# Performance work log

Hardware: AMD Instinct MI355X
Metric: run time of the kernel (lower is better)

## Reference

```python
import jax, jax.numpy as jnp
import numpy as np

B, T, H, W = 2, 4, 32, 32
DINO_DIM, COG_DIM, NUM_HEADS = 768, 1920, 12
HEAD_DIM = DINO_DIM // NUM_HEADS


def _layernorm(x, g, b, eps=1e-5):
    mu = jnp.mean(x, axis=-1, keepdims=True)
    var = jnp.mean(jnp.square(x - mu), axis=-1, keepdims=True)
    return (x - mu) * jax.lax.rsqrt(var + eps) * g + b


def setup_inputs() -> dict:
    key = jax.random.key(0)
    ks = jax.random.split(key, 12)
    s_d = 1.0 / np.sqrt(DINO_DIM)
    s_c = 1.0 / np.sqrt(COG_DIM)
    return {
        "dino_query": jax.random.normal(ks[0], (B, DINO_DIM, H, W), jnp.float32),
        "cogvideo_keys": jax.random.normal(ks[1], (B, T, H, W, COG_DIM), jnp.float32),
        "temporal_weights": jax.random.uniform(ks[2], (T,), jnp.float32),
        "Wq": jax.random.normal(ks[3], (DINO_DIM, DINO_DIM), jnp.float32) * s_d,
        "bq": jnp.zeros((DINO_DIM,), jnp.float32),
        "Wk": jax.random.normal(ks[4], (COG_DIM, DINO_DIM), jnp.float32) * s_c,
        "bk": jnp.zeros((DINO_DIM,), jnp.float32),
        "Wv": jax.random.normal(ks[5], (COG_DIM, DINO_DIM), jnp.float32) * s_c,
        "bv": jnp.zeros((DINO_DIM,), jnp.float32),
        "Wo": jax.random.normal(ks[6], (DINO_DIM, DINO_DIM), jnp.float32) * s_d,
        "bo": jnp.zeros((DINO_DIM,), jnp.float32),
        "gq": jnp.ones((DINO_DIM,), jnp.float32),
        "Bq": jnp.zeros((DINO_DIM,), jnp.float32),
        "gkv": jnp.ones((COG_DIM,), jnp.float32),
        "Bkv": jnp.zeros((COG_DIM,), jnp.float32),
    }


def reference(dino_query, cogvideo_keys, temporal_weights,
              Wq, bq, Wk, bk, Wv, bv, Wo, bo, gq, Bq, gkv, Bkv):
    b, c, h, w = dino_query.shape
    t = cogvideo_keys.shape[1]
    hw, tkv = h * w, t * cogvideo_keys.shape[2] * cogvideo_keys.shape[3]

    # [B,C,H,W] -> [B,H,W,C]; project after LayerNorm
    xq = _layernorm(jnp.transpose(dino_query, (0, 2, 3, 1)), gq, Bq)
    xkv = _layernorm(cogvideo_keys, gkv, Bkv)
    q = xq @ Wq + bq                      # [B,H,W,C]
    k = xkv @ Wk + bk                     # [B,T,Hk,Wk,C]
    v = xkv @ Wv + bv

    q = q.reshape(b, hw, NUM_HEADS, HEAD_DIM).transpose(0, 2, 1, 3)    # [B,nh,HW,hd]
    k = k.reshape(b, tkv, NUM_HEADS, HEAD_DIM).transpose(0, 2, 1, 3)   # [B,nh,TKV,hd]
    v = v.reshape(b, tkv, NUM_HEADS, HEAD_DIM).transpose(0, 2, 1, 3)

    scores = jnp.einsum('bnqd,bnkd->bnqk', q, k) / np.sqrt(HEAD_DIM)   # [B,nh,HW,TKV]
    # per-key temporal weight: each of the T frames contributes HW keys
    w_key = jnp.repeat(temporal_weights, tkv // t)                     # [TKV]
    scores = scores * w_key[None, None, None, :]
    probs = jax.nn.softmax(scores, axis=-1)

    out = jnp.einsum('bnqk,bnkd->bnqd', probs, v)                      # [B,nh,HW,hd]
    out = out.transpose(0, 2, 1, 3).reshape(b, h, w, c)
    out = out @ Wo + bo
    return jnp.transpose(out, (0, 3, 1, 2))                            # [B,C,H,W]
```

## Files before the change

kernel.cpp:

```cpp
#include <hip/hip_runtime.h>
#include <hip/hip_bf16.h>
#include <math.h>

#define BB   2
#define HWl  1024
#define DINO 768
#define COG  1920
#define NHh  12
#define TKV  4096
#define MQ   (BB*HWl)
#define MKV  (BB*TKV)
#define NSPL 4
#define ROWS_PER_SPLIT (BB*NHh*HWl)

typedef __attribute__((ext_vector_type(8))) short bf16x8;
typedef __attribute__((ext_vector_type(4))) float f32x4;

__device__ __forceinline__ unsigned short f2bf_bits(float f) {
    __hip_bfloat16 h = __float2bfloat16(f);
    return *reinterpret_cast<unsigned short*>(&h);
}

__device__ __forceinline__ void glds16(const __hip_bfloat16* g, __hip_bfloat16* l) {
    __builtin_amdgcn_global_load_lds((const __attribute__((address_space(1))) void*)g,
                                     (__attribute__((address_space(3))) void*)l, 16, 0, 0);
}

__global__ void transpose_dino(const float* __restrict__ x, float* __restrict__ y) {
    int h0 = blockIdx.x * 64, c0 = blockIdx.y * 64, b = blockIdx.z;
    __shared__ float T[64][65];
    #pragma unroll
    for (int i = 0; i < 16; ++i) {
        int idx = threadIdx.x + i * 256;
        int c = idx >> 6, h = idx & 63;
        T[c][h] = x[((size_t)b * DINO + c0 + c) * HWl + h0 + h];
    }
    __syncthreads();
    #pragma unroll
    for (int i = 0; i < 16; ++i) {
        int idx = threadIdx.x + i * 256;
        int r = idx >> 6, c = idx & 63;
        y[((size_t)b * HWl + h0 + r) * DINO + c0 + c] = T[c][r];
    }
}

template<int W, int NC>
__global__ void ln_rows_w(const float* __restrict__ x, const float* __restrict__ g,
                          const float* __restrict__ be, __hip_bfloat16* __restrict__ y) {
    const int W4 = W >> 2;
    int row = blockIdx.x * 4 + (threadIdx.x >> 6);
    int lane = threadIdx.x & 63;
    const float4* xr = (const float4*)(x + (size_t)row * W);
    const float4* g4 = (const float4*)g;
    const float4* b4 = (const float4*)be;
    float4 v[NC];
    float s = 0.f, ss = 0.f;
    #pragma unroll
    for (int i = 0; i < NC; ++i) {
        int c = lane + i * 64;
        float4 t = (c < W4) ? xr[c] : (float4){0.f, 0.f, 0.f, 0.f};
        v[i] = t;
        s  += t.x + t.y + t.z + t.w;
        ss += t.x * t.x + t.y * t.y + t.z * t.z + t.w * t.w;
    }
    #pragma unroll
    for (int off = 1; off < 64; off <<= 1) {
        s  += __shfl_xor(s, off);
        ss += __shfl_xor(ss, off);
    }
    float mu = s / W;
    float rstd = rsqrtf(ss / W - mu * mu + 1e-5f);
    ushort4* yr = (ushort4*)(y + (size_t)row * W);
    #pragma unroll
    for (int i = 0; i < NC; ++i) {
        int c = lane + i * 64;
        if (c < W4) {
            float4 t = v[i];
            float4 gg = g4[c], bb = b4[c];
            ushort4 o;
            o.x = f2bf_bits((t.x - mu) * rstd * gg.x + bb.x);
            o.y = f2bf_bits((t.y - mu) * rstd * gg.y + bb.y);
            o.z = f2bf_bits((t.z - mu) * rstd * gg.z + bb.z);
            o.w = f2bf_bits((t.w - mu) * rstd * gg.w + bb.w);
            yr[c] = o;
        }
    }
}

__global__ void wt_trans(const float* __restrict__ Wq, const float* __restrict__ Wk,
                         const float* __restrict__ Wv, const float* __restrict__ Wo,
                         __hip_bfloat16* WqT, __hip_bfloat16* WkvT, __hip_bfloat16* WoT) {
    int mid = blockIdx.z;
    const float* src = (mid == 0) ? Wq : (mid == 1) ? Wk : (mid == 2) ? Wv : Wo;
    __hip_bfloat16* dst;
    int rowoff = 0;
    if (mid == 0) dst = WqT;
    else if (mid == 1) dst = WkvT;
    else if (mid == 2) { dst = WkvT; rowoff = 768; }
    else dst = WoT;
    int K = (mid == 1 || mid == 2) ? COG : DINO;
    int k0 = blockIdx.x * 32;
    if (k0 >= K) return;
    int n0 = blockIdx.y * 32;
    __shared__ float T[32][33];
    #pragma unroll
    for (int i = 0; i < 4; ++i) {
        int idx = threadIdx.x + i * 256;
        int r = idx >> 5, c = idx & 31;
        T[r][c] = src[(size_t)(k0 + r) * DINO + n0 + c];
    }
    __syncthreads();
    #pragma unroll
    for (int i = 0; i < 4; ++i) {
        int idx = threadIdx.x + i * 256;
        int r = idx >> 5, c = idx & 31;
        dst[(size_t)(rowoff + n0 + r) * K + k0 + c] = __float2bfloat16(T[c][r]);
    }
}

__global__ __launch_bounds__(256) void gemm_kv(const __hip_bfloat16* __restrict__ A,
                                               const __hip_bfloat16* __restrict__ Bt,
                                               const float* __restrict__ bk,
                                               const float* __restrict__ bv,
                                               __hip_bfloat16* __restrict__ kb,
                                               __hip_bfloat16* __restrict__ VT) {
    const int K = COG;
    __shared__ __hip_bfloat16 As[128 * 64];
    __shared__ __hip_bfloat16 Bs[128 * 64];
    int m0 = blockIdx.x * 128, n0 = blockIdx.y * 128;
    int tid = threadIdx.x, w = tid >> 6, lane = tid & 63;
    int l4 = lane & 15, lq = lane >> 4;
    int mq = (w & 1) * 64, nq = (w >> 1) * 64;
    f32x4 acc[4][4];
    #pragma unroll
    for (int i = 0; i < 4; ++i)
        #pragma unroll
        for (int j = 0; j < 4; ++j) acc[i][j] = (f32x4){0.f, 0.f, 0.f, 0.f};

    int rr = tid >> 3;
    int gc = (tid & 7) ^ (rr & 7);
    const __hip_bfloat16* ag = A  + (size_t)(m0 + rr) * K + gc * 8;
    const __hip_bfloat16* bg = Bt + (size_t)(n0 + rr) * K + gc * 8;
    __hip_bfloat16* asl = As + (w * 8) * 64;
    __hip_bfloat16* bsl = Bs + (w * 8) * 64;
    int sws = l4 & 7;

    for (int k0 = 0; k0 < K; k0 += 64) {
        __syncthreads();
        #pragma unroll
        for (int g = 0; g < 4; ++g) {
            glds16(ag + (size_t)(g * 32) * K + k0, asl + g * 32 * 64);
            glds16(bg + (size_t)(g * 32) * K + k0, bsl + g * 32 * 64);
        }
        __syncthreads();
        #pragma unroll
        for (int h = 0; h < 2; ++h) {
            bf16x8 a[4], b[4];
            #pragma unroll
            for (int i = 0; i < 4; ++i)
                a[i] = *(const bf16x8*)(As + (mq + 16 * i + l4) * 64 + (((h * 4 + lq) ^ sws) * 8));
            #pragma unroll
            for (int j = 0; j < 4; ++j)
                b[j] = *(const bf16x8*)(Bs + (nq + 16 * j + l4) * 64 + (((h * 4 + lq) ^ sws) * 8));
            #pragma unroll
            for (int i = 0; i < 4; ++i)
                #pragma unroll
                for (int j = 0; j < 4; ++j)
                    acc[i][j] = __builtin_amdgcn_mfma_f32_16x16x32_bf16(a[i], b[j], acc[i][j], 0, 0, 0);
        }
    }

    if (n0 < 768) {
        #pragma unroll
        for (int i = 0; i < 4; ++i)
            #pragma unroll
            for (int j = 0; j < 4; ++j)
                #pragma unroll
                for (int r = 0; r < 4; ++r) {
                    int m = m0 + mq + 16 * i + lq * 4 + r;
                    int n = n0 + nq + 16 * j + l4;
                    kb[(size_t)m * DINO + n] = __float2bfloat16(acc[i][j][r] + bk[n]);
                }
    } else {
        #pragma unroll
        for (int i = 0; i < 4; ++i)
            #pragma unroll
            for (int j = 0; j < 4; ++j)
                #pragma unroll
                for (int r = 0; r < 4; ++r) {
                    int m = m0 + mq + 16 * i + lq * 4 + r;
                    int n = n0 + nq + 16 * j + l4 - 768;
                    VT[((size_t)((m >> 12) * 768 + n)) * TKV + (m & 4095)] =
                        __float2bfloat16(acc[i][j][r] + bv[n]);
                }
    }
}

template<bool ONCHW>
__global__ __launch_bounds__(256) void gemm_qo(const __hip_bfloat16* __restrict__ A,
                                               const __hip_bfloat16* __restrict__ Bt,
                                               const float* __restrict__ bias,
                                               void* __restrict__ outp) {
    const int K = DINO;
    __shared__ __hip_bfloat16 As[64 * 64];
    __shared__ __hip_bfloat16 Bs[128 * 64];
    int m0 = blockIdx.x * 64, n0 = blockIdx.y * 128;
    int tid = threadIdx.x, w = tid >> 6, lane = tid & 63;
    int l4 = lane & 15, lq = lane >> 4;
    int mq = (w & 1) * 32, nq = (w >> 1) * 64;
    f32x4 acc[2][4];
    #pragma unroll
    for (int i = 0; i < 2; ++i)
        #pragma unroll
        for (int j = 0; j < 4; ++j) acc[i][j] = (f32x4){0.f, 0.f, 0.f, 0.f};

    int rr = tid >> 3;
    int gc = (tid & 7) ^ (rr & 7);
    const __hip_bfloat16* ag = A  + (size_t)(m0 + rr) * K + gc * 8;
    const __hip_bfloat16* bg = Bt + (size_t)(n0 + rr) * K + gc * 8;
    __hip_bfloat16* asl = As + (w * 8) * 64;
    __hip_bfloat16* bsl = Bs + (w * 8) * 64;
    int sws = l4 & 7;

    for (int k0 = 0; k0 < K; k0 += 64) {
        __syncthreads();
        #pragma unroll
        for (int g = 0; g < 2; ++g)
            glds16(ag + (size_t)(g * 32) * K + k0, asl + g * 32 * 64);
        #pragma unroll
        for (int g = 0; g < 4; ++g)
            glds16(bg + (size_t)(g * 32) * K + k0, bsl + g * 32 * 64);
        __syncthreads();
        #pragma unroll
        for (int h = 0; h < 2; ++h) {
            bf16x8 a[2], b[4];
            #pragma unroll
            for (int i = 0; i < 2; ++i)
                a[i] = *(const bf16x8*)(As + (mq + 16 * i + l4) * 64 + (((h * 4 + lq) ^ sws) * 8));
            #pragma unroll
            for (int j = 0; j < 4; ++j)
                b[j] = *(const bf16x8*)(Bs + (nq + 16 * j + l4) * 64 + (((h * 4 + lq) ^ sws) * 8));
            #pragma unroll
            for (int i = 0; i < 2; ++i)
                #pragma unroll
                for (int j = 0; j < 4; ++j)
                    acc[i][j] = ONCHW
                      ? __builtin_amdgcn_mfma_f32_16x16x32_bf16(b[j], a[i], acc[i][j], 0, 0, 0)
                      : __builtin_amdgcn_mfma_f32_16x16x32_bf16(a[i], b[j], acc[i][j], 0, 0, 0);
        }
    }

    if (!ONCHW) {
        __hip_bfloat16* out = (__hip_bfloat16*)outp;
        #pragma unroll
        for (int i = 0; i < 2; ++i)
            #pragma unroll
            for (int j = 0; j < 4; ++j)
                #pragma unroll
                for (int r = 0; r < 4; ++r) {
                    int m = m0 + mq + 16 * i + lq * 4 + r;
                    int n = n0 + nq + 16 * j + l4;
                    out[(size_t)m * DINO + n] = __float2bfloat16(acc[i][j][r] + bias[n]);
                }
    } else {
        float* out = (float*)outp;
        #pragma unroll
        for (int i = 0; i < 2; ++i)
            #pragma unroll
            for (int j = 0; j < 4; ++j)
                #pragma unroll
                for (int r = 0; r < 4; ++r) {
                    int n = n0 + nq + 16 * j + lq * 4 + r;
                    int m = m0 + mq + 16 * i + l4;
                    int b = m >> 10, hw = m & 1023;
                    out[((size_t)b * DINO + n) * HWl + hw] = acc[i][j][r] + bias[n];
                }
    }
}

__global__ __launch_bounds__(256) void attn3(const __hip_bfloat16* __restrict__ qb,
                                             const __hip_bfloat16* __restrict__ kb,
                                             const __hip_bfloat16* __restrict__ VT,
                                             const float* __restrict__ tw,
                                             float* __restrict__ Opart,
                                             float* __restrict__ lpart) {
    int bid = blockIdx.x;
    int g = bid % 96, qc = bid / 96;
    int s = g & 3, bh = g >> 2;
    int head = bh % NHh, b = bh / NHh;
    int tid = threadIdx.x, w = tid >> 6, lane = tid & 63;
    int l4 = lane & 15, lq = lane >> 4;

    __shared__ __hip_bfloat16 Ks[64 * 64];
    __shared__ __hip_bfloat16 Vs[64 * 64];
    __shared__ __hip_bfloat16 Ps[4 * 32 * 64];

    const __hip_bfloat16* qbase = qb + (size_t)(b * HWl + qc * 128 + w * 32 + l4) * DINO + head * 64;
    bf16x8 qA0 = *(const bf16x8*)(qbase + lq * 8);
    bf16x8 qA1 = *(const bf16x8*)(qbase + 32 + lq * 8);
    const __hip_bfloat16* qbase2 = qbase + (size_t)16 * DINO;
    bf16x8 qB0 = *(const bf16x8*)(qbase2 + lq * 8);
    bf16x8 qB1 = *(const bf16x8*)(qbase2 + 32 + lq * 8);

    float c = tw[s] * 0.125f * 1.44269504f;
    float l_iA = 0.f, l_iB = 0.f;
    f32x4 oA[4], oB[4];
    #pragma unroll
    for (int j = 0; j < 4; ++j) { oA[j] = (f32x4){0.f,0.f,0.f,0.f}; oB[j] = (f32x4){0.f,0.f,0.f,0.f}; }

    int rowA = w * 16 + (lane >> 3);
    int cg = (lane & 7) ^ ((lane >> 3) & 7);
    const __hip_bfloat16* kg0 = kb + (size_t)(b * TKV + s * 1024 + rowA) * DINO + head * 64 + cg * 8;
    const __hip_bfloat16* kg1 = kg0 + (size_t)8 * DINO;
    const __hip_bfloat16* vg0 = VT + (size_t)(b * 768 + head * 64 + rowA) * TKV + s * 1024 + cg * 8;
    const __hip_bfloat16* vg1 = vg0 + (size_t)8 * TKV;
    __hip_bfloat16* kl0 = Ks + (w * 2 + 0) * 512;
    __hip_bfloat16* kl1 = Ks + (w * 2 + 1) * 512;
    __hip_bfloat16* vl0 = Vs + (w * 2 + 0) * 512;
    __hip_bfloat16* vl1 = Vs + (w * 2 + 1) * 512;

    int sw0 = (lq ^ (l4 & 7)) * 8;
    int sw1 = ((4 + lq) ^ (l4 & 7)) * 8;
    __hip_bfloat16* PsA = Ps + w * 2048 + l4 * 64;
    __hip_bfloat16* PsB = Ps + w * 2048 + (16 + l4) * 64;

    for (int kt = 0; kt < 16; ++kt) {
        __syncthreads();
        glds16(kg0 + (size_t)kt * 64 * DINO, kl0);
        glds16(kg1 + (size_t)kt * 64 * DINO, kl1);
        glds16(vg0 + kt * 64, vl0);
        glds16(vg1 + kt * 64, vl1);
        __syncthreads();

        f32x4 stA[4], stB[4];
        #pragma unroll
        for (int j = 0; j < 4; ++j) {
            const __hip_bfloat16* kr = Ks + (16 * j + l4) * 64;
            bf16x8 kf0 = *(const bf16x8*)(kr + sw0);
            bf16x8 kf1 = *(const bf16x8*)(kr + sw1);
            f32x4 a = (f32x4){0.f,0.f,0.f,0.f};
            a = __builtin_amdgcn_mfma_f32_16x16x32_bf16(kf0, qA0, a, 0, 0, 0);
            a = __builtin_amdgcn_mfma_f32_16x16x32_bf16(kf1, qA1, a, 0, 0, 0);
            stA[j] = a;
            f32x4 bb = (f32x4){0.f,0.f,0.f,0.f};
            bb = __builtin_amdgcn_mfma_f32_16x16x32_bf16(kf0, qB0, bb, 0, 0, 0);
            bb = __builtin_amdgcn_mfma_f32_16x16x32_bf16(kf1, qB1, bb, 0, 0, 0);
            stB[j] = bb;
        }

        float lsA = 0.f, lsB = 0.f;
        #pragma unroll
        for (int j = 0; j < 4; ++j)
            #pragma unroll
            for (int r = 0; r < 4; ++r) {
                float eA = exp2f(stA[j][r] * c);
                float eB = exp2f(stB[j][r] * c);
                stA[j][r] = eA; lsA += eA;
                stB[j][r] = eB; lsB += eB;
            }
        lsA += __shfl_xor(lsA, 16); lsA += __shfl_xor(lsA, 32);
        lsB += __shfl_xor(lsB, 16); lsB += __shfl_xor(lsB, 32);
        l_iA += lsA; l_iB += lsB;

        #pragma unroll
        for (int j = 0; j < 4; ++j) {
            int off = (((2 * j + (lq >> 1)) ^ (l4 & 7)) << 3) + (lq & 1) * 4;
            ushort4 pA, pB;
            pA.x = f2bf_bits(stA[j][0]); pA.y = f2bf_bits(stA[j][1]);
            pA.z = f2bf_bits(stA[j][2]); pA.w = f2bf_bits(stA[j][3]);
            pB.x = f2bf_bits(stB[j][0]); pB.y = f2bf_bits(stB[j][1]);
            pB.z = f2bf_bits(stB[j][2]); pB.w = f2bf_bits(stB[j][3]);
            *(ushort4*)&PsA[off] = pA;
            *(ushort4*)&PsB[off] = pB;
        }
        bf16x8 paA0 = *(const bf16x8*)(PsA + sw0);
        bf16x8 paA1 = *(const bf16x8*)(PsA + sw1);
        bf16x8 paB0 = *(const bf16x8*)(PsB + sw0);
        bf16x8 paB1 = *(const bf16x8*)(PsB + sw1);

        #pragma unroll
        for (int j = 0; j < 4; ++j) {
            const __hip_bfloat16* vr = Vs + (16 * j + l4) * 64;
            bf16x8 vf0 = *(const bf16x8*)(vr + sw0);
            bf16x8 vf1 = *(const bf16x8*)(vr + sw1);
            oA[j] = __builtin_amdgcn_mfma_f32_16x16x32_bf16(paA0, vf0, oA[j], 0, 0, 0);
            oA[j] = __builtin_amdgcn_mfma_f32_16x16x32_bf16(paA1, vf1, oA[j], 0, 0, 0);
            oB[j] = __builtin_amdgcn_mfma_f32_16x16x32_bf16(paB0, vf0, oB[j], 0, 0, 0);
            oB[j] = __builtin_amdgcn_mfma_f32_16x16x32_bf16(paB1, vf1, oB[j], 0, 0, 0);
        }
    }

    size_t rb = (size_t)s * ROWS_PER_SPLIT + (size_t)(b * NHh + head) * HWl + qc * 128 + w * 32;
    #pragma unroll
    for (int j = 0; j < 4; ++j)
        #pragma unroll
        for (int r = 0; r < 4; ++r) {
            Opart[(rb + lq * 4 + r) * 64 + j * 16 + l4]      = oA[j][r];
            Opart[(rb + 16 + lq * 4 + r) * 64 + j * 16 + l4] = oB[j][r];
        }
    if (lq == 0) {
        lpart[rb + l4]      = l_iA;
        lpart[rb + 16 + l4] = l_iB;
    }
}

__global__ void combine(const float* __restrict__ Opart, const float* __restrict__ lpart,
                        __hip_bfloat16* __restrict__ attn) {
    int p = blockIdx.x * 4 + (threadIdx.x >> 6);
    int d = threadIdx.x & 63;
    float L = 0.f, O = 0.f;
    #pragma unroll
    for (int s = 0; s < NSPL; ++s) {
        L += lpart[(size_t)s * ROWS_PER_SPLIT + p];
        O += Opart[((size_t)s * ROWS_PER_SPLIT + p) * 64 + d];
    }
    float res = O / L;
    int q = p & 1023;
    int bh = p >> 10;
    int head = bh % NHh, b = bh / NHh;
    attn[((size_t)(b * HWl + q)) * DINO + head * 64 + d] = __float2bfloat16(res);
}

extern "C" void kernel_launch(void* const* d_in, const int* in_sizes, int n_in,
                              void* d_out, int out_size, void* d_ws, size_t ws_size,
                              hipStream_t stream) {
    (void)in_sizes; (void)n_in; (void)out_size; (void)ws_size;
    const float* dino = (const float*)d_in[0];
    const float* cog  = (const float*)d_in[1];
    const float* tw   = (const float*)d_in[2];
    const float* Wq   = (const float*)d_in[3];
    const float* bq   = (const float*)d_in[4];
    const float* Wk   = (const float*)d_in[5];
    const float* bk   = (const float*)d_in[6];
    const float* Wv   = (const float*)d_in[7];
    const float* bv   = (const float*)d_in[8];
    const float* Wo   = (const float*)d_in[9];
    const float* bo   = (const float*)d_in[10];
    const float* gq   = (const float*)d_in[11];
    const float* Bq   = (const float*)d_in[12];
    const float* gkv  = (const float*)d_in[13];
    const float* Bkv  = (const float*)d_in[14];

    char* p = (char*)d_ws;
    float* xqT = (float*)p;                    p += (size_t)MQ * DINO * 4;
    __hip_bfloat16* xq = (__hip_bfloat16*)p;   p += (size_t)MQ * DINO * 2;
    char* alias = p;                           p += (size_t)MKV * COG * 2;
    __hip_bfloat16* xkv = (__hip_bfloat16*)alias;
    __hip_bfloat16* WqT  = (__hip_bfloat16*)p; p += (size_t)DINO * DINO * 2;
    __hip_bfloat16* WkvT = (__hip_bfloat16*)p; p += (size_t)1536 * COG * 2;
    __hip_bfloat16* WoT  = (__hip_bfloat16*)p; p += (size_t)DINO * DINO * 2;
    __hip_bfloat16* qb   = (__hip_bfloat16*)p; p += (size_t)MQ  * DINO * 2;
    __hip_bfloat16* kb   = (__hip_bfloat16*)p; p += (size_t)MKV * DINO * 2;
    __hip_bfloat16* VT   = (__hip_bfloat16*)p; p += (size_t)MKV * DINO * 2;
    __hip_bfloat16* attnb = (__hip_bfloat16*)p; p += (size_t)MQ * DINO * 2;
    float* Opart = (float*)alias;
    float* lpart = (float*)(alias + (size_t)NSPL * ROWS_PER_SPLIT * 64 * 4);

    transpose_dino<<<dim3(16, 12, 2), 256, 0, stream>>>(dino, xqT);
    ln_rows_w<DINO, 3><<<MQ / 4,  256, 0, stream>>>(xqT, gq, Bq, xq);
    ln_rows_w<COG,  8><<<MKV / 4, 256, 0, stream>>>(cog, gkv, Bkv, xkv);
    wt_trans<<<dim3(60, 24, 4), 256, 0, stream>>>(Wq, Wk, Wv, Wo, WqT, WkvT, WoT);

    gemm_qo<false><<<dim3(32, 6), 256, 0, stream>>>(xq, WqT, bq, qb);
    gemm_kv<<<dim3(64, 12), 256, 0, stream>>>(xkv, WkvT, bk, bv, kb, VT);

    attn3<<<BB * NHh * 8 * NSPL, 256, 0, stream>>>(qb, kb, VT, tw, Opart, lpart);
    combine<<<ROWS_PER_SPLIT / 4, 256, 0, stream>>>(Opart, lpart, attnb);

    gemm_qo<true><<<dim3(32, 6), 256, 0, stream>>>(attnb, WoT, bo, d_out);
}
```

Baseline: 295.7 us.

## Merge preprocessing kernels and fuse Q and KV projections into single launches

Combines the dino transpose, both LayerNorms and the weight transposes into one heterogeneous prep kernel, and computes the dino LayerNorm directly from NCHW layout, which removes the fp32 transposed intermediate buffer. The Q projection and the KV projection GEMMs are merged into one stage1 launch whose block ranges take different tile shapes. The intent is to cut launch count and the extra fp32 round trip, and to let the small Q GEMM fill idle CUs alongside the KV GEMM. In exchange, the branchy kernels share one LDS allocation and register budget, and the NCHW LayerNorm reads each strided column twice.

```diff
diff --git a/kernel.cpp b/kernel.cpp
--- a/kernel.cpp
+++ b/kernel.cpp
@@ -26,181 +26,271 @@
                                      (__attribute__((address_space(3))) void*)l, 16, 0, 0);
 }
 
-__global__ void transpose_dino(const float* __restrict__ x, float* __restrict__ y) {
-    int h0 = blockIdx.x * 64, c0 = blockIdx.y * 64, b = blockIdx.z;
-    __shared__ float T[64][65];
-    #pragma unroll
-    for (int i = 0; i < 16; ++i) {
-        int idx = threadIdx.x + i * 256;
-        int c = idx >> 6, h = idx & 63;
-        T[c][h] = x[((size_t)b * DINO + c0 + c) * HWl + h0 + h];
+__global__ __launch_bounds__(256) void prep(const float* __restrict__ dino,
+                                            const float* __restrict__ cog,
+                                            const float* __restrict__ gq,  const float* __restrict__ Bq,
+                                            const float* __restrict__ gkv, const float* __restrict__ Bkv,
+                                            const float* __restrict__ Wq, const float* __restrict__ Wk,
+                                            const float* __restrict__ Wv, const float* __restrict__ Wo,
+                                            __hip_bfloat16* __restrict__ xq,
+                                            __hip_bfloat16* __restrict__ xkv,
+                                            __hip_bfloat16* WqT, __hip_bfloat16* WkvT, __hip_bfloat16* WoT) {
+    int bid = blockIdx.x, tid = threadIdx.x;
+    if (bid < 2048) {
+        const int W = COG, W4 = W >> 2, NC = 8;
+        int row = bid * 4 + (tid >> 6), lane = tid & 63;
+        const float4* xr = (const float4*)(cog + (size_t)row * W);
+        const float4* g4 = (const float4*)gkv;
+        const float4* b4 = (const float4*)Bkv;
+        float4 v[NC];
+        float s = 0.f, ss = 0.f;
+        #pragma unroll
+        for (int i = 0; i < NC; ++i) {
+            int c = lane + i * 64;
+            float4 t = (c < W4) ? xr[c] : (float4){0.f, 0.f, 0.f, 0.f};
+            v[i] = t;
+            s  += t.x + t.y + t.z + t.w;
+            ss += t.x * t.x + t.y * t.y + t.z * t.z + t.w * t.w;
+        }
+        #pragma unroll
+        for (int off = 1; off < 64; off <<= 1) {
+            s  += __shfl_xor(s, off);
+            ss += __shfl_xor(ss, off);
+        }
+        float mu = s / W;
+        float rstd = rsqrtf(ss / W - mu * mu + 1e-5f);
+        ushort4* yr = (ushort4*)(xkv + (size_t)row * W);
+        #pragma unroll
+        for (int i = 0; i < NC; ++i) {
+            int c = lane + i * 64;
+            if (c < W4) {
+                float4 t = v[i];
+                float4 gg = g4[c], bb = b4[c];
+                ushort4 o;
+                o.x = f2bf_bits((t.x - mu) * rstd * gg.x + bb.x);
+                o.y = f2bf_bits((t.y - mu) * rstd * gg.y + bb.y);
+                o.z = f2bf_bits((t.z - mu) * rstd * gg.z + bb.z);
+                o.w = f2bf_bits((t.w - mu) * rstd * gg.w + bb.w);
+                yr[c] = o;
+            }
+        }
+    } else if (bid < 2080) {
+        int t = bid - 2048;
+        int b = t >> 4, hw0 = (t & 15) << 6;
+        int hw = tid & 63, cq = tid >> 6;
+        const float* base = dino + (size_t)b * (DINO * HWl) + hw0 + hw;
+        float s = 0.f, ss = 0.f;
+        for (int c = cq; c < DINO; c += 4) {
+            float v = base[(size_t)c * HWl];
+            s += v; ss += v * v;
+        }
+        __shared__ float sred[4][64], ssred[4][64];
+        sred[cq][hw] = s; ssred[cq][hw] = ss;
+        __syncthreads();
+        __shared__ float mu_s[64], rs_s[64];
+        if (tid < 64) {
+            float S  = sred[0][tid] + sred[1][tid] + sred[2][tid] + sred[3][tid];
+            float SS = ssred[0][tid] + ssred[1][tid] + ssred[2][tid] + ssred[3][tid];
+            float mu = S * (1.f / DINO);
+            mu_s[tid] = mu;
+            rs_s[tid] = rsqrtf(SS * (1.f / DINO) - mu * mu + 1e-5f);
+        }
+        __syncthreads();
+        float mu = mu_s[hw], rs = rs_s[hw];
+        __shared__ __hip_bfloat16 T2[64][68];
+        for (int ch = 0; ch < 12; ++ch) {
+            __syncthreads();
+            #pragma unroll
+            for (int i = 0; i < 16; ++i) {
+                int cl = cq + 4 * i;
+                int c = ch * 64 + cl;
+                float v = base[(size_t)c * HWl];
+                T2[hw][cl] = __float2bfloat16((v - mu) * rs * gq[c] + Bq[c]);
+            }
+            __syncthreads();
+            int cl = (tid & 15) * 4;
+            int hr = tid >> 4;
+            #pragma unroll
+            for (int ii = 0; ii < 4; ++ii) {
+                int hwr = hr + ii * 16;
+                *(ushort4*)(xq + (size_t)(b * HWl + hw0 + hwr) * DINO + ch * 64 + cl) =
+                    *(ushort4*)&T2[hwr][cl];
+            }
+        }
+    } else {
+        int bid2 = bid - 2080;
+        int mid = bid2 / 1440, r = bid2 % 1440;
+        int k0 = (r % 60) * 32, n0 = (r / 60) * 32;
+        const float* src = (mid == 0) ? Wq : (mid == 1) ? Wk : (mid == 2) ? Wv : Wo;
+        __hip_bfloat16* dst;
+        int rowoff = 0;
+        if (mid == 0) dst = WqT;
+        else if (mid == 1) dst = WkvT;
+        else if (mid == 2) { dst = WkvT; rowoff = 768; }
+        else dst = WoT;
+        int K = (mid == 1 || mid == 2) ? COG : DINO;
+        if (k0 >= K) return;
+        __shared__ float T[32][33];
+        #pragma unroll
+        for (int i = 0; i < 4; ++i) {
+            int idx = tid + i * 256;
+            int rr = idx >> 5, c = idx & 31;
+            T[rr][c] = src[(size_t)(k0 + rr) * DINO + n0 + c];
+        }
+        __syncthreads();
+        #pragma unroll
+        for (int i = 0; i < 4; ++i) {
+            int idx = tid + i * 256;
+            int rr = idx >> 5, c = idx & 31;
+            dst[(size_t)(rowoff + n0 + rr) * K + k0 + c] = __float2bfloat16(T[c][rr]);
+        }
     }
-    __syncthreads();
-    #pragma unroll
-    for (int i = 0; i < 16; ++i) {
-        int idx = threadIdx.x + i * 256;
-        int r = idx >> 6, c = idx & 63;
-        y[((size_t)b * HWl + h0 + r) * DINO + c0 + c] = T[c][r];
-    }
-}
-
-template<int W, int NC>
-__global__ void ln_rows_w(const float* __restrict__ x, const float* __restrict__ g,
-                          const float* __restrict__ be, __hip_bfloat16* __restrict__ y) {
-    const int W4 = W >> 2;
-    int row = blockIdx.x * 4 + (threadIdx.x >> 6);
-    int lane = threadIdx.x & 63;
-    const float4* xr = (const float4*)(x + (size_t)row * W);
-    const float4* g4 = (const float4*)g;
-    const float4* b4 = (const float4*)be;
-    float4 v[NC];
-    float s = 0.f, ss = 0.f;
-    #pragma unroll
-    for (int i = 0; i < NC; ++i) {
-        int c = lane + i * 64;
-        float4 t = (c < W4) ? xr[c] : (float4){0.f, 0.f, 0.f, 0.f};
-        v[i] = t;
-        s  += t.x + t.y + t.z + t.w;
-        ss += t.x * t.x + t.y * t.y + t.z * t.z + t.w * t.w;
-    }
-    #pragma unroll
-    for (int off = 1; off < 64; off <<= 1) {
-        s  += __shfl_xor(s, off);
-        ss += __shfl_xor(ss, off);
-    }
-    float mu = s / W;
-    float rstd = rsqrtf(ss / W - mu * mu + 1e-5f);
-    ushort4* yr = (ushort4*)(y + (size_t)row * W);
-    #pragma unroll
-    for (int i = 0; i < NC; ++i) {
-        int c = lane + i * 64;
-        if (c < W4) {
-            float4 t = v[i];
-            float4 gg = g4[c], bb = b4[c];
-            ushort4 o;
-            o.x = f2bf_bits((t.x - mu) * rstd * gg.x + bb.x);
-            o.y = f2bf_bits((t.y - mu) * rstd * gg.y + bb.y);
-            o.z = f2bf_bits((t.z - mu) * rstd * gg.z + bb.z);
-            o.w = f2bf_bits((t.w - mu) * rstd * gg.w + bb.w);
-            yr[c] = o;
-        }
-    }
-}
-
-__global__ void wt_trans(const float* __restrict__ Wq, const float* __restrict__ Wk,
-                         const float* __restrict__ Wv, const float* __restrict__ Wo,
-                         __hip_bfloat16* WqT, __hip_bfloat16* WkvT, __hip_bfloat16* WoT) {
-    int mid = blockIdx.z;
-    const float* src = (mid == 0) ? Wq : (mid == 1) ? Wk : (mid == 2) ? Wv : Wo;
-    __hip_bfloat16* dst;
-    int rowoff = 0;
-    if (mid == 0) dst = WqT;
-    else if (mid == 1) dst = WkvT;
-    else if (mid == 2) { dst = WkvT; rowoff = 768; }
-    else dst = WoT;
-    int K = (mid == 1 || mid == 2) ? COG : DINO;
-    int k0 = blockIdx.x * 32;
-    if (k0 >= K) return;
-    int n0 = blockIdx.y * 32;
-    __shared__ float T[32][33];
-    #pragma unroll
-    for (int i = 0; i < 4; ++i) {
-        int idx = threadIdx.x + i * 256;
-        int r = idx >> 5, c = idx & 31;
-        T[r][c] = src[(size_t)(k0 + r) * DINO + n0 + c];
-    }
-    __syncthreads();
-    #pragma unroll
-    for (int i = 0; i < 4; ++i) {
-        int idx = threadIdx.x + i * 256;
-        int r = idx >> 5, c = idx & 31;
-        dst[(size_t)(rowoff + n0 + r) * K + k0 + c] = __float2bfloat16(T[c][r]);
-    }
-}
-
-__global__ __launch_bounds__(256) void gemm_kv(const __hip_bfloat16* __restrict__ A,
-                                               const __hip_bfloat16* __restrict__ Bt,
-                                               const float* __restrict__ bk,
-                                               const float* __restrict__ bv,
-                                               __hip_bfloat16* __restrict__ kb,
-                                               __hip_bfloat16* __restrict__ VT) {
-    const int K = COG;
-    __shared__ __hip_bfloat16 As[128 * 64];
-    __shared__ __hip_bfloat16 Bs[128 * 64];
-    int m0 = blockIdx.x * 128, n0 = blockIdx.y * 128;
+}
+
+__global__ __launch_bounds__(256) void stage1(const __hip_bfloat16* __restrict__ xq,
+                                              const __hip_bfloat16* __restrict__ WqT,
+                                              const float* __restrict__ bq,
+                                              __hip_bfloat16* __restrict__ qb,
+                                              const __hip_bfloat16* __restrict__ xkv,
+                                              const __hip_bfloat16* __restrict__ WkvT,
+                                              const float* __restrict__ bk,
+                                              const float* __restrict__ bv,
+                                              __hip_bfloat16* __restrict__ kb,
+                                              __hip_bfloat16* __restrict__ VT) {
+    __shared__ __hip_bfloat16 SM[2 * 128 * 64];
+    int bid = blockIdx.x;
     int tid = threadIdx.x, w = tid >> 6, lane = tid & 63;
     int l4 = lane & 15, lq = lane >> 4;
-    int mq = (w & 1) * 64, nq = (w >> 1) * 64;
-    f32x4 acc[4][4];
-    #pragma unroll
-    for (int i = 0; i < 4; ++i)
-        #pragma unroll
-        for (int j = 0; j < 4; ++j) acc[i][j] = (f32x4){0.f, 0.f, 0.f, 0.f};
-
+    int sws = l4 & 7;
     int rr = tid >> 3;
-    int gc = (tid & 7) ^ (rr & 7);
-    const __hip_bfloat16* ag = A  + (size_t)(m0 + rr) * K + gc * 8;
-    const __hip_bfloat16* bg = Bt + (size_t)(n0 + rr) * K + gc * 8;
-    __hip_bfloat16* asl = As + (w * 8) * 64;
-    __hip_bfloat16* bsl = Bs + (w * 8) * 64;
-    int sws = l4 & 7;
-
-    for (int k0 = 0; k0 < K; k0 += 64) {
-        __syncthreads();
-        #pragma unroll
-        for (int g = 0; g < 4; ++g) {
-            glds16(ag + (size_t)(g * 32) * K + k0, asl + g * 32 * 64);
-            glds16(bg + (size_t)(g * 32) * K + k0, bsl + g * 32 * 64);
-        }
-        __syncthreads();
-        #pragma unroll
-        for (int h = 0; h < 2; ++h) {
-            bf16x8 a[4], b[4];
+    int gcs = (tid & 7) ^ (rr & 7);
+
+    if (bid < 768) {
+        const int K = COG;
+        __hip_bfloat16* As = SM;
+        __hip_bfloat16* Bs = SM + 128 * 64;
+        int m0 = (bid & 63) * 128, n0 = (bid >> 6) * 128;
+        int mq = (w & 1) * 64, nq = (w >> 1) * 64;
+        f32x4 acc[4][4];
+        #pragma unroll
+        for (int i = 0; i < 4; ++i)
+            #pragma unroll
+            for (int j = 0; j < 4; ++j) acc[i][j] = (f32x4){0.f, 0.f, 0.f, 0.f};
+
+        const __hip_bfloat16* ag = xkv  + (size_t)(m0 + rr) * K + gcs * 8;
+        const __hip_bfloat16* bg = WkvT + (size_t)(n0 + rr) * K + gcs * 8;
+        __hip_bfloat16* asl = As + (w * 8) * 64;
+        __hip_bfloat16* bsl = Bs + (w * 8) * 64;
+
+        for (int k0 = 0; k0 < K; k0 += 64) {
+            __syncthreads();
+            #pragma unroll
+            for (int g = 0; g < 4; ++g) {
+                glds16(ag + (size_t)(g * 32) * K + k0, asl + g * 32 * 64);
+                glds16(bg + (size_t)(g * 32) * K + k0, bsl + g * 32 * 64);
+            }
+            __syncthreads();
+            #pragma unroll
+            for (int h = 0; h < 2; ++h) {
+                bf16x8 a[4], b[4];
+                #pragma unroll
+                for (int i = 0; i < 4; ++i)
+                    a[i] = *(const bf16x8*)(As + (mq + 16 * i + l4) * 64 + (((h * 4 + lq) ^ sws) * 8));
+                #pragma unroll
+                for (int j = 0; j < 4; ++j)
+                    b[j] = *(const bf16x8*)(Bs + (nq + 16 * j + l4) * 64 + (((h * 4 + lq) ^ sws) * 8));
+                #pragma unroll
+                for (int i = 0; i < 4; ++i)
+                    #pragma unroll
+                    for (int j = 0; j < 4; ++j)
+                        acc[i][j] = __builtin_amdgcn_mfma_f32_16x16x32_bf16(a[i], b[j], acc[i][j], 0, 0, 0);
+            }
+        }
+
+        if (n0 < 768) {
             #pragma unroll
             for (int i = 0; i < 4; ++i)
-                a[i] = *(const bf16x8*)(As + (mq + 16 * i + l4) * 64 + (((h * 4 + lq) ^ sws) * 8));
-            #pragma unroll
-            for (int j = 0; j < 4; ++j)
-                b[j] = *(const bf16x8*)(Bs + (nq + 16 * j + l4) * 64 + (((h * 4 + lq) ^ sws) * 8));
+                #pragma unroll
+                for (int j = 0; j < 4; ++j)
+                    #pragma unroll
+                    for (int r = 0; r < 4; ++r) {
+                        int m = m0 + mq + 16 * i + lq * 4 + r;
+                        int n = n0 + nq + 16 * j + l4;
+                        kb[(size_t)m * DINO + n] = __float2bfloat16(acc[i][j][r] + bk[n]);
+                    }
+        } else {
             #pragma unroll
             for (int i = 0; i < 4; ++i)
                 #pragma unroll
                 for (int j = 0; j < 4; ++j)
-                    acc[i][j] = __builtin_amdgcn_mfma_f32_16x16x32_bf16(a[i], b[j], acc[i][j], 0, 0, 0);
-        }
-    }
-
-    if (n0 < 768) {
-        #pragma unroll
-        for (int i = 0; i < 4; ++i)
+                    #pragma unroll
+                    for (int r = 0; r < 4; ++r) {
+                        int m = m0 + mq + 16 * i + lq * 4 + r;
+                        int n = n0 + nq + 16 * j + l4 - 768;
+                        VT[((size_t)((m >> 12) * 768 + n)) * TKV + (m & 4095)] =
+                            __float2bfloat16(acc[i][j][r] + bv[n]);
+                    }
+        }
+    } else {
+        const int K = DINO;
+        __hip_bfloat16* As = SM;
+        __hip_bfloat16* Bs = SM + 64 * 64;
+        int bid2 = bid - 768;
+        int m0 = (bid2 & 31) * 64, n0 = (bid2 >> 5) * 128;
+        int mq = (w & 1) * 32, nq = (w >> 1) * 64;
+        f32x4 acc[2][4];
+        #pragma unroll
+        for (int i = 0; i < 2; ++i)
+            #pragma unroll
+            for (int j = 0; j < 4; ++j) acc[i][j] = (f32x4){0.f, 0.f, 0.f, 0.f};
+
+        const __hip_bfloat16* ag = xq  + (size_t)(m0 + rr) * K + gcs * 8;
+        const __hip_bfloat16* bg = WqT + (size_t)(n0 + rr) * K + gcs * 8;
+        __hip_bfloat16* asl = As + (w * 8) * 64;
+        __hip_bfloat16* bsl = Bs + (w * 8) * 64;
+
+        for (int k0 = 0; k0 < K; k0 += 64) {
+            __syncthreads();
+            #pragma unroll
+            for (int g = 0; g < 2; ++g)
+                glds16(ag + (size_t)(g * 32) * K + k0, asl + g * 32 * 64);
+            #pragma unroll
+            for (int g = 0; g < 4; ++g)
+                glds16(bg + (size_t)(g * 32) * K + k0, bsl + g * 32 * 64);
+            __syncthreads();
+            #pragma unroll
+            for (int h = 0; h < 2; ++h) {
+                bf16x8 a[2], b[4];
+                #pragma unroll
+                for (int i = 0; i < 2; ++i)
+                    a[i] = *(const bf16x8*)(As + (mq + 16 * i + l4) * 64 + (((h * 4 + lq) ^ sws) * 8));
+                #pragma unroll
+                for (int j = 0; j < 4; ++j)
+                    b[j] = *(const bf16x8*)(Bs + (nq + 16 * j + l4) * 64 + (((h * 4 + lq) ^ sws) * 8));
+                #pragma unroll
+                for (int i = 0; i < 2; ++i)
+                    #pragma unroll
+                    for (int j = 0; j < 4; ++j)
+                        acc[i][j] = __builtin_amdgcn_mfma_f32_16x16x32_bf16(a[i], b[j], acc[i][j], 0, 0, 0);
+            }
+        }
+        #pragma unroll
+        for (int i = 0; i < 2; ++i)
             #pragma unroll
             for (int j = 0; j < 4; ++j)
                 #pragma unroll
                 for (int r = 0; r < 4; ++r) {
                     int m = m0 + mq + 16 * i + lq * 4 + r;
                     int n = n0 + nq + 16 * j + l4;
-                    kb[(size_t)m * DINO + n] = __float2bfloat16(acc[i][j][r] + bk[n]);
-                }
-    } else {
-        #pragma unroll
-        for (int i = 0; i < 4; ++i)
-            #pragma unroll
-            for (int j = 0; j < 4; ++j)
-                #pragma unroll
-                for (int r = 0; r < 4; ++r) {
-                    int m = m0 + mq + 16 * i + lq * 4 + r;
-                    int n = n0 + nq + 16 * j + l4 - 768;
-                    VT[((size_t)((m >> 12) * 768 + n)) * TKV + (m & 4095)] =
-                        __float2bfloat16(acc[i][j][r] + bv[n]);
+                    qb[(size_t)m * DINO + n] = __float2bfloat16(acc[i][j][r] + bq[n]);
                 }
     }
 }
 
-template<bool ONCHW>
-__global__ __launch_bounds__(256) void gemm_qo(const __hip_bfloat16* __restrict__ A,
-                                               const __hip_bfloat16* __restrict__ Bt,
-                                               const float* __restrict__ bias,
-                                               void* __restrict__ outp) {
+__global__ __launch_bounds__(256) void gemm_o(const __hip_bfloat16* __restrict__ A,
+                                              const __hip_bfloat16* __restrict__ Bt,
+                                              const float* __restrict__ bias,
+                                              float* __restrict__ out) {
     const int K = DINO;
     __shared__ __hip_bfloat16 As[64 * 64];
     __shared__ __hip_bfloat16 Bs[128 * 64];
@@ -244,38 +334,20 @@
             for (int i = 0; i < 2; ++i)
                 #pragma unroll
                 for (int j = 0; j < 4; ++j)
-                    acc[i][j] = ONCHW
-                      ? __builtin_amdgcn_mfma_f32_16x16x32_bf16(b[j], a[i], acc[i][j], 0, 0, 0)
-                      : __builtin_amdgcn_mfma_f32_16x16x32_bf16(a[i], b[j], acc[i][j], 0, 0, 0);
+                    acc[i][j] = __builtin_amdgcn_mfma_f32_16x16x32_bf16(b[j], a[i], acc[i][j], 0, 0, 0);
         }
     }
-
-    if (!ONCHW) {
-        __hip_bfloat16* out = (__hip_bfloat16*)outp;
-        #pragma unroll
-        for (int i = 0; i < 2; ++i)
-            #pragma unroll
-            for (int j = 0; j < 4; ++j)
-                #pragma unroll
-                for (int r = 0; r < 4; ++r) {
-                    int m = m0 + mq + 16 * i + lq * 4 + r;
-                    int n = n0 + nq + 16 * j + l4;
-                    out[(size_t)m * DINO + n] = __float2bfloat16(acc[i][j][r] + bias[n]);
-                }
-    } else {
-        float* out = (float*)outp;
-        #pragma unroll
-        for (int i = 0; i < 2; ++i)
-            #pragma unroll
-            for (int j = 0; j < 4; ++j)
-                #pragma unroll
-                for (int r = 0; r < 4; ++r) {
-                    int n = n0 + nq + 16 * j + lq * 4 + r;
-                    int m = m0 + mq + 16 * i + l4;
-                    int b = m >> 10, hw = m & 1023;
-                    out[((size_t)b * DINO + n) * HWl + hw] = acc[i][j][r] + bias[n];
-                }
-    }
+    #pragma unroll
+    for (int i = 0; i < 2; ++i)
+        #pragma unroll
+        for (int j = 0; j < 4; ++j)
+            #pragma unroll
+            for (int r = 0; r < 4; ++r) {
+                int n = n0 + nq + 16 * j + lq * 4 + r;
+                int m = m0 + mq + 16 * i + l4;
+                int b = m >> 10, hw = m & 1023;
+                out[((size_t)b * DINO + n) * HWl + hw] = acc[i][j][r] + bias[n];
+            }
 }
 
 __global__ __launch_bounds__(256) void attn3(const __hip_bfloat16* __restrict__ qb,
@@ -442,7 +514,6 @@
     const float* Bkv  = (const float*)d_in[14];
 
     char* p = (char*)d_ws;
-    float* xqT = (float*)p;                    p += (size_t)MQ * DINO * 4;
     __hip_bfloat16* xq = (__hip_bfloat16*)p;   p += (size_t)MQ * DINO * 2;
     char* alias = p;                           p += (size_t)MKV * COG * 2;
     __hip_bfloat16* xkv = (__hip_bfloat16*)alias;
@@ -456,16 +527,10 @@
     float* Opart = (float*)alias;
     float* lpart = (float*)(alias + (size_t)NSPL * ROWS_PER_SPLIT * 64 * 4);
 
-    transpose_dino<<<dim3(16, 12, 2), 256, 0, stream>>>(dino, xqT);
-    ln_rows_w<DINO, 3><<<MQ / 4,  256, 0, stream>>>(xqT, gq, Bq, xq);
-    ln_rows_w<COG,  8><<<MKV / 4, 256, 0, stream>>>(cog, gkv, Bkv, xkv);
-    wt_trans<<<dim3(60, 24, 4), 256, 0, stream>>>(Wq, Wk, Wv, Wo, WqT, WkvT, WoT);
-
-    gemm_qo<false><<<dim3(32, 6), 256, 0, stream>>>(xq, WqT, bq, qb);
-    gemm_kv<<<dim3(64, 12), 256, 0, stream>>>(xkv, WkvT, bk, bv, kb, VT);
-
+    prep<<<7840, 256, 0, stream>>>(dino, cog, gq, Bq, gkv, Bkv,
+                                   Wq, Wk, Wv, Wo, xq, xkv, WqT, WkvT, WoT);
+    stage1<<<960, 256, 0, stream>>>(xq, WqT, bq, qb, xkv, WkvT, bk, bv, kb, VT);
     attn3<<<BB * NHh * 8 * NSPL, 256, 0, stream>>>(qb, kb, VT, tw, Opart, lpart);
     combine<<<ROWS_PER_SPLIT / 4, 256, 0, stream>>>(Opart, lpart, attnb);
-
-    gemm_qo<true><<<dim3(32, 6), 256, 0, stream>>>(attnb, WoT, bo, d_out);
-}
+    gemm_o<<<dim3(32, 6), 256, 0, stream>>>(attnb, WoT, bo, (float*)d_out);
+}
```

Result: slower. 361.1 us (+22.1%).
